# Optimization experiments

Hardware: AMD Instinct MI355X
Metric: run time of the kernel (lower is better)

Reference implementation:

```python
import jax, jax.numpy as jnp
import numpy as np

U, I, D, K, L, E = 100000, 50000, 64, 128, 2, 1250000
N = U + I
EPS = 1e-12


def setup_inputs() -> dict:
    key = jax.random.key(0)
    ks = jax.random.split(key, 8)
    return {
        "user_emb": jax.random.normal(ks[0], (U, D), jnp.float32) * 0.1,
        "item_emb": jax.random.normal(ks[1], (I, D), jnp.float32) * 0.1,
        "user_intent": jax.random.normal(ks[2], (D, K), jnp.float32) * 0.1,
        "item_intent": jax.random.normal(ks[3], (D, K), jnp.float32) * 0.1,
        "adj_vals": jax.random.uniform(ks[4], (E,), jnp.float32) * 0.1,
        "h_idx": jax.random.randint(ks[5], (E,), 0, N, jnp.int32),
        "t_idx": jax.random.randint(ks[6], (E,), 0, N, jnp.int32),
        "users": jax.random.randint(ks[7], (1024,), 0, U, jnp.int32),
        "items": jax.random.randint(jax.random.fold_in(key, 9), (1024,), 0, I, jnp.int32),
    }


def _l2norm(x):
    # torch F.normalize(p=2, dim=1): x / max(||x||_2, eps)
    n = jnp.sqrt(jnp.sum(x * x, axis=1, keepdims=True))
    return x / jnp.maximum(n, EPS)


def reference(user_emb, item_emb, user_intent, item_intent, adj_vals, h_idx, t_idx, users, items):
    n_users = user_emb.shape[0]
    n_nodes = n_users + item_emb.shape[0]

    def spmm(vals, x):
        # sparse [N,N] @ dense [N,D] via edge gather + segment-sum scatter
        return jax.ops.segment_sum(vals[:, None] * x[t_idx], h_idx, num_segments=n_nodes)

    def adaptive_vals(head, tail):
        hn, tn = _l2norm(head), _l2norm(tail)
        edge_alpha = (jnp.sum(hn * tn, axis=1) + 1.0) * 0.5  # [E]
        row_sum = jax.ops.segment_sum(edge_alpha, h_idx, num_segments=n_nodes)  # dense row-sum equivalent
        d_inv = jnp.where(row_sum > 0, 1.0 / row_sum, 0.0)
        return d_inv[h_idx] * edge_alpha  # G edge values

    all_emb = [jnp.concatenate([user_emb, item_emb], axis=0)]  # [N, D]
    gnn_list, int_list, gaa_list, iaa_list = [], [], [], []
    for _ in range(L):
        ek = all_emb[-1]
        gnn = spmm(adj_vals, ek)
        u_e, i_e = ek[:n_users], ek[n_users:]
        u_int = jax.nn.softmax(u_e @ user_intent, axis=1) @ user_intent.T
        i_int = jax.nn.softmax(i_e @ item_intent, axis=1) @ item_intent.T
        intl = jnp.concatenate([u_int, i_int], axis=0)
        g_graph = adaptive_vals(gnn[h_idx], gnn[t_idx])
        g_inten = adaptive_vals(intl[h_idx], intl[t_idx])
        gaa = spmm(g_graph, ek)
        iaa = spmm(g_inten, ek)
        gnn_list.append(gnn); int_list.append(intl)
        gaa_list.append(gaa); iaa_list.append(iaa)
        all_emb.append(gnn + intl + gaa + iaa + ek)

    final = jnp.sum(jnp.stack(all_emb, axis=1), axis=1)  # [N, D]
    ua, ia = final[:n_users], final[n_users:]
    return (ua, ia, jnp.stack(gnn_list), jnp.stack(int_list), jnp.stack(gaa_list), jnp.stack(iaa_list))
```

## Files before the change

### kernel.cpp

```cpp
#include <hip/hip_runtime.h>


#define U_CNT 100000
#define I_CNT 50000
#define D_DIM 64
#define K_DIM 128
#define L_LAYERS 2
#define E_CNT 1250000
#define N_CNT (U_CNT + I_CNT)
#define EPSF 1e-12f

#define UBLK ((U_CNT + 63) / 64)
#define IBLK ((I_CNT + 63) / 64)

#define SC_BLOCKS 256
#define SC_TPB 256
#define SC_CHUNK ((N_CNT + SC_BLOCKS - 1) / SC_BLOCKS)

typedef float vfloat4 __attribute__((ext_vector_type(4)));

__device__ __forceinline__ void nt_store4(float* p, float4 v) {
  vfloat4 nv;
  nv.x = v.x;
  nv.y = v.y;
  nv.z = v.z;
  nv.w = v.w;
  __builtin_nontemporal_store(nv, (vfloat4*)p);
}

__global__ void init_kernel(const float* __restrict__ ue, const float* __restrict__ ie,
                            float* __restrict__ ek) {
  int idx = blockIdx.x * blockDim.x + threadIdx.x;
  const int total = N_CNT * D_DIM;
  for (; idx < total; idx += gridDim.x * blockDim.x) {
    float v = (idx < U_CNT * D_DIM) ? ue[idx] : ie[idx - U_CNT * D_DIM];
    ek[idx] = v;
  }
}

__global__ void hist_kernel(const int* __restrict__ h_idx, int* __restrict__ counts) {
  int e = blockIdx.x * blockDim.x + threadIdx.x;
  for (; e < E_CNT; e += gridDim.x * blockDim.x) atomicAdd(&counts[h_idx[e]], 1);
}

__global__ void scanA_kernel(const int* __restrict__ counts, int* __restrict__ partial) {
  int b = blockIdx.x, tid = threadIdx.x, lane = tid & 63, wv = tid >> 6;
  int lo = b * SC_CHUNK;
  int hi = lo + SC_CHUNK;
  if (hi > N_CNT) hi = N_CNT;
  int s = 0;
  for (int i = lo + tid; i < hi; i += SC_TPB) s += counts[i];
#pragma unroll
  for (int off = 32; off > 0; off >>= 1) s += __shfl_xor(s, off, 64);
  __shared__ int ws[4];
  if (lane == 0) ws[wv] = s;
  __syncthreads();
  if (tid == 0) partial[b] = ws[0] + ws[1] + ws[2] + ws[3];
}

__global__ void scanB_kernel(const int* __restrict__ partial, int* __restrict__ offs) {
  int tid = threadIdx.x, lane = tid & 63, wv = tid >> 6;
  int v = partial[tid];
  int x = v;
#pragma unroll
  for (int off = 1; off < 64; off <<= 1) {
    int y = __shfl_up(x, off, 64);
    if (lane >= off) x += y;
  }
  __shared__ int wt[4];
  if (lane == 63) wt[wv] = x;
  __syncthreads();
  int add = 0;
  for (int w = 0; w < wv; w++) add += wt[w];
  offs[tid] = add + x - v;
}

__global__ void scanC_kernel(const int* __restrict__ counts, const int* __restrict__ offs,
                             int* __restrict__ row_ptr, int* __restrict__ cursor) {
  int b = blockIdx.x, tid = threadIdx.x, lane = tid & 63, wv = tid >> 6;
  __shared__ int wt[4];
  int lo = b * SC_CHUNK;
  int hi = lo + SC_CHUNK;
  if (hi > N_CNT) hi = N_CNT;
  int carry = offs[b];
  for (int base = lo; base < hi; base += SC_TPB) {
    int i = base + tid;
    int v = (i < hi) ? counts[i] : 0;
    int x = v;
#pragma unroll
    for (int off = 1; off < 64; off <<= 1) {
      int y = __shfl_up(x, off, 64);
      if (lane >= off) x += y;
    }
    if (lane == 63) wt[wv] = x;
    __syncthreads();
    int add = carry;
    for (int w = 0; w < wv; w++) add += wt[w];
    if (i < hi) {
      int e = add + x - v;
      row_ptr[i] = e;
      cursor[i] = e;
    }
    int tot = wt[0] + wt[1] + wt[2] + wt[3];
    __syncthreads();
    carry += tot;
  }
  if (b == 0 && tid == 0) row_ptr[N_CNT] = E_CNT;
}

__global__ void scatter_kernel(const int* __restrict__ h_idx, const int* __restrict__ t_idx,
                               const float* __restrict__ adj_vals, int* __restrict__ cursor,
                               int* __restrict__ t_sorted, float* __restrict__ v_sorted) {
  int e = blockIdx.x * blockDim.x + threadIdx.x;
  for (; e < E_CNT; e += gridDim.x * blockDim.x) {
    int h = h_idx[e];
    int pos = atomicAdd(&cursor[h], 1);
    t_sorted[pos] = t_idx[e];
    v_sorted[pos] = adj_vals[e];
  }
}

__global__ void transposeW_kernel(const float* __restrict__ Wu, const float* __restrict__ Wi,
                                  float* __restrict__ WuT, float* __restrict__ WiT) {
  int idx = blockIdx.x * blockDim.x + threadIdx.x;
  for (; idx < 2 * D_DIM * K_DIM; idx += gridDim.x * blockDim.x) {
    int w = idx >> 13, r = idx & (D_DIM * K_DIM - 1);
    int d = r >> 7, k = r & (K_DIM - 1);
    const float* W = w ? Wi : Wu;
    float* WT = w ? WiT : WuT;
    WT[k * D_DIM + d] = W[d * K_DIM + k];
  }
}

__global__ void spmm_gnn_kernel(const float* __restrict__ ek, const int* __restrict__ t_sorted,
                                const float* __restrict__ v_sorted,
                                const int* __restrict__ row_ptr, float* __restrict__ gnn,
                                float* __restrict__ invn_g) {
  int wv = threadIdx.x >> 6, lane = threadIdx.x & 63;
  int slot = lane >> 4, f = (lane & 15) << 2;
  int n = blockIdx.x * 4 + wv;
  if (n >= N_CNT) return;
  int start = row_ptr[n], end = row_ptr[n + 1];
  float ax = 0.f, ay = 0.f, az = 0.f, aw = 0.f;
  for (int i = start; i < end; i += 4) {
    int idx = i + slot;
    int ic = (idx < end) ? idx : (end - 1);
    int t = t_sorted[ic];
    float v = v_sorted[ic];
    if (idx >= end) v = 0.f;
    const float4 x = *(const float4*)(ek + (size_t)t * D_DIM + f);
    ax = fmaf(v, x.x, ax);
    ay = fmaf(v, x.y, ay);
    az = fmaf(v, x.z, az);
    aw = fmaf(v, x.w, aw);
  }
#pragma unroll
  for (int off = 16; off <= 32; off <<= 1) {
    ax += __shfl_xor(ax, off, 64);
    ay += __shfl_xor(ay, off, 64);
    az += __shfl_xor(az, off, 64);
    aw += __shfl_xor(aw, off, 64);
  }
  if (slot == 0) {
    float4 o = make_float4(ax, ay, az, aw);
    *(float4*)(gnn + (size_t)n * D_DIM + f) = o;
  }
  float ss = ax * ax + ay * ay + az * az + aw * aw;
#pragma unroll
  for (int off = 1; off <= 8; off <<= 1) ss += __shfl_xor(ss, off, 64);
  if (lane == 0) invn_g[n] = 1.f / fmaxf(sqrtf(ss), EPSF);
}

__global__ __launch_bounds__(256, 4) void intent_kernel(
    const float* __restrict__ ek, const float* __restrict__ Wu, const float* __restrict__ WuT,
    const float* __restrict__ Wi, const float* __restrict__ WiT, float* __restrict__ intl,
    float* __restrict__ invn_i) {
  __shared__ float buf[K_DIM * 65];
  const int tid = threadIdx.x;
  const int tx = tid & 15, ty = tid >> 4;
  const int b = blockIdx.x;
  int n0, cnt;
  const float *W, *WT;
  if (b < UBLK) {
    n0 = b * 64;
    cnt = (U_CNT - n0 < 64) ? (U_CNT - n0) : 64;
    W = Wu;
    WT = WuT;
  } else {
    n0 = U_CNT + (b - UBLK) * 64;
    cnt = (N_CNT - n0 < 64) ? (N_CNT - n0) : 64;
    W = Wi;
    WT = WiT;
  }

#pragma unroll
  for (int it = 0; it < 4; it++) {
    int idx = tid + 256 * it;
    int r = idx >> 4, q = idx & 15;
    float4 v = make_float4(0.f, 0.f, 0.f, 0.f);
    if (r < cnt) v = *(const float4*)(ek + (size_t)(n0 + r) * D_DIM + q * 4);
    buf[r * 65 + 4 * q + 0] = v.x;
    buf[r * 65 + 4 * q + 1] = v.y;
    buf[r * 65 + 4 * q + 2] = v.z;
    buf[r * 65 + 4 * q + 3] = v.w;
  }
  __syncthreads();

  float a[4][8];
#pragma unroll
  for (int i = 0; i < 4; i++)
#pragma unroll
    for (int j = 0; j < 8; j++) a[i][j] = 0.f;

  const float* wp = W + 8 * tx;
  float4 w0 = *(const float4*)(wp);
  float4 w1 = *(const float4*)(wp + 4);
  for (int d = 0; d < D_DIM; d++) {
    float4 nw0, nw1;
    if (d < D_DIM - 1) {
      nw0 = *(const float4*)(wp + (d + 1) * K_DIM);
      nw1 = *(const float4*)(wp + (d + 1) * K_DIM + 4);
    }
    float e0 = buf[(4 * ty + 0) * 65 + d];
    float e1 = buf[(4 * ty + 1) * 65 + d];
    float e2 = buf[(4 * ty + 2) * 65 + d];
    float e3 = buf[(4 * ty + 3) * 65 + d];
    float wv[8] = {w0.x, w0.y, w0.z, w0.w, w1.x, w1.y, w1.z, w1.w};
    float ev[4] = {e0, e1, e2, e3};
#pragma unroll
    for (int i = 0; i < 4; i++)
#pragma unroll
      for (int j = 0; j < 8; j++) a[i][j] = fmaf(ev[i], wv[j], a[i][j]);
    w0 = nw0;
    w1 = nw1;
  }

  float mx[4], sm[4], inv_s[4];
#pragma unroll
  for (int i = 0; i < 4; i++) {
    float m = a[i][0];
#pragma unroll
    for (int j = 1; j < 8; j++) m = fmaxf(m, a[i][j]);
    mx[i] = m;
  }
#pragma unroll
  for (int off = 1; off <= 8; off <<= 1)
#pragma unroll
    for (int i = 0; i < 4; i++) mx[i] = fmaxf(mx[i], __shfl_xor(mx[i], off, 64));
#pragma unroll
  for (int i = 0; i < 4; i++) {
    float s = 0.f;
#pragma unroll
    for (int j = 0; j < 8; j++) {
      a[i][j] = __expf(a[i][j] - mx[i]);
      s += a[i][j];
    }
    sm[i] = s;
  }
#pragma unroll
  for (int off = 1; off <= 8; off <<= 1)
#pragma unroll
    for (int i = 0; i < 4; i++) sm[i] += __shfl_xor(sm[i], off, 64);
#pragma unroll
  for (int i = 0; i < 4; i++) inv_s[i] = 1.f / sm[i];

  __syncthreads();
#pragma unroll
  for (int i = 0; i < 4; i++)
#pragma unroll
    for (int j = 0; j < 8; j++) buf[(8 * tx + j) * 65 + 4 * ty + i] = a[i][j];
  __syncthreads();

  float o[4][4];
#pragma unroll
  for (int i = 0; i < 4; i++)
#pragma unroll
    for (int j = 0; j < 4; j++) o[i][j] = 0.f;

  const float* wtp = WT + 4 * tx;
  float4 t0 = *(const float4*)(wtp);
  for (int k = 0; k < K_DIM; k++) {
    float4 nt;
    if (k < K_DIM - 1) nt = *(const float4*)(wtp + (k + 1) * D_DIM);
    float p0 = buf[k * 65 + 4 * ty + 0];
    float p1 = buf[k * 65 + 4 * ty + 1];
    float p2 = buf[k * 65 + 4 * ty + 2];
    float p3 = buf[k * 65 + 4 * ty + 3];
    float pv[4] = {p0, p1, p2, p3};
    float tv[4] = {t0.x, t0.y, t0.z, t0.w};
#pragma unroll
    for (int i = 0; i < 4; i++)
#pragma unroll
      for (int j = 0; j < 4; j++) o[i][j] = fmaf(pv[i], tv[j], o[i][j]);
    t0 = nt;
  }

  float ns[4];
#pragma unroll
  for (int i = 0; i < 4; i++) {
    float s = 0.f;
#pragma unroll
    for (int j = 0; j < 4; j++) {
      o[i][j] *= inv_s[i];
      s = fmaf(o[i][j], o[i][j], s);
    }
    ns[i] = s;
  }
#pragma unroll
  for (int off = 1; off <= 8; off <<= 1)
#pragma unroll
    for (int i = 0; i < 4; i++) ns[i] += __shfl_xor(ns[i], off, 64);
  if (tx == 0) {
#pragma unroll
    for (int i = 0; i < 4; i++) {
      int r = 4 * ty + i;
      if (r < cnt) invn_i[n0 + r] = 1.f / fmaxf(sqrtf(ns[i]), EPSF);
    }
  }
#pragma unroll
  for (int i = 0; i < 4; i++) {
    int r = 4 * ty + i;
    if (r < cnt) {
      float4 v = make_float4(o[i][0], o[i][1], o[i][2], o[i][3]);
      *(float4*)(intl + (size_t)(n0 + r) * D_DIM + 4 * tx) = v;
    }
  }
}

template <bool LAST>
__global__ void passB_kernel(const float* __restrict__ ek, const float* __restrict__ gnn,
                             const float* __restrict__ intl, const float* __restrict__ invn_g,
                             const float* __restrict__ invn_i, const int* __restrict__ t_sorted,
                             const int* __restrict__ row_ptr, float* __restrict__ gaa,
                             float* __restrict__ iaa, float* __restrict__ ek_next,
                             const float* __restrict__ ek0, float* __restrict__ fin) {
  int wv = threadIdx.x >> 6, lane = threadIdx.x & 63;
  int slot = lane >> 4, f = (lane & 15) << 2;
  int n = blockIdx.x * 4 + wv;
  if (n >= N_CNT) return;
  int start = row_ptr[n], end = row_ptr[n + 1];
  const float4 gh = *(const float4*)(gnn + (size_t)n * D_DIM + f);
  const float4 ih = *(const float4*)(intl + (size_t)n * D_DIM + f);
  float ig = invn_g[n], ii = invn_i[n];
  float rs_g = 0.f, rs_i = 0.f;
  float gx = 0.f, gy = 0.f, gz = 0.f, gw = 0.f;
  float ix = 0.f, iy = 0.f, iz = 0.f, iw = 0.f;
  for (int i = start; i < end; i += 4) {
    int idx = i + slot;
    int ic = (idx < end) ? idx : (end - 1);
    int t = t_sorted[ic];
    size_t rb = (size_t)t * D_DIM + f;
    const float4 gt = *(const float4*)(gnn + rb);
    const float4 it = *(const float4*)(intl + rb);
    const float4 et = *(const float4*)(ek + rb);
    float ivg = invn_g[t];
    float ivi = invn_i[t];
    float dg = gh.x * gt.x + gh.y * gt.y + gh.z * gt.z + gh.w * gt.w;
    float di = ih.x * it.x + ih.y * it.y + ih.z * it.z + ih.w * it.w;
#pragma unroll
    for (int off = 1; off <= 8; off <<= 1) {
      dg += __shfl_xor(dg, off, 64);
      di += __shfl_xor(di, off, 64);
    }
    float ag = fmaf(dg * ig, ivg, 1.f) * 0.5f;
    float ai = fmaf(di * ii, ivi, 1.f) * 0.5f;
    if (idx >= end) { ag = 0.f; ai = 0.f; }
    rs_g += ag;
    rs_i += ai;
    gx = fmaf(ag, et.x, gx);
    gy = fmaf(ag, et.y, gy);
    gz = fmaf(ag, et.z, gz);
    gw = fmaf(ag, et.w, gw);
    ix = fmaf(ai, et.x, ix);
    iy = fmaf(ai, et.y, iy);
    iz = fmaf(ai, et.z, iz);
    iw = fmaf(ai, et.w, iw);
  }
#pragma unroll
  for (int off = 16; off <= 32; off <<= 1) {
    rs_g += __shfl_xor(rs_g, off, 64);
    rs_i += __shfl_xor(rs_i, off, 64);
    gx += __shfl_xor(gx, off, 64);
    gy += __shfl_xor(gy, off, 64);
    gz += __shfl_xor(gz, off, 64);
    gw += __shfl_xor(gw, off, 64);
    ix += __shfl_xor(ix, off, 64);
    iy += __shfl_xor(iy, off, 64);
    iz += __shfl_xor(iz, off, 64);
    iw += __shfl_xor(iw, off, 64);
  }
  float dgi = (rs_g > 0.f) ? 1.f / rs_g : 0.f;
  float dii = (rs_i > 0.f) ? 1.f / rs_i : 0.f;
  if (slot == 0) {
    size_t ob = (size_t)n * D_DIM + f;
    float4 ga = make_float4(gx * dgi, gy * dgi, gz * dgi, gw * dgi);
    float4 ia = make_float4(ix * dii, iy * dii, iz * dii, iw * dii);
    nt_store4(gaa + ob, ga);
    nt_store4(iaa + ob, ia);
    const float4 eh = *(const float4*)(ek + ob);
    float4 en = make_float4(gh.x + ih.x + ga.x + ia.x + eh.x, gh.y + ih.y + ga.y + ia.y + eh.y,
                            gh.z + ih.z + ga.z + ia.z + eh.z, gh.w + ih.w + ga.w + ia.w + eh.w);
    if (LAST) {
      const float4 e0 = *(const float4*)(ek0 + ob);
      float4 fo = make_float4(e0.x + eh.x + en.x, e0.y + eh.y + en.y, e0.z + eh.z + en.z,
                              e0.w + eh.w + en.w);
      nt_store4(fin + ob, fo);
    } else {
      *(float4*)(ek_next + ob) = en;
    }
  }
}

extern "C" void kernel_launch(void* const* d_in, const int* in_sizes, int n_in, void* d_out,
                              int out_size, void* d_ws, size_t ws_size, hipStream_t stream) {
  const float* user_emb = (const float*)d_in[0];
  const float* item_emb = (const float*)d_in[1];
  const float* user_intent = (const float*)d_in[2];
  const float* item_intent = (const float*)d_in[3];
  const float* adj_vals = (const float*)d_in[4];
  const int* h_idx = (const int*)d_in[5];
  const int* t_idx = (const int*)d_in[6];

  float* out = (float*)d_out;
  float* fin = out;
  float* gnn_base = out + (size_t)N_CNT * D_DIM;
  float* intl_base = gnn_base + (size_t)L_LAYERS * N_CNT * D_DIM;
  float* gaa_base = intl_base + (size_t)L_LAYERS * N_CNT * D_DIM;
  float* iaa_base = gaa_base + (size_t)L_LAYERS * N_CNT * D_DIM;

  float* ws = (float*)d_ws;
  float* ekA = ws;
  float* ekB = ekA + (size_t)N_CNT * D_DIM;
  float* ekC = ekB + (size_t)N_CNT * D_DIM;
  float* v_sorted = ekC + (size_t)N_CNT * D_DIM;
  float* invn_g = v_sorted + E_CNT;
  float* invn_i = invn_g + N_CNT;
  int* t_sorted = (int*)(invn_i + N_CNT);
  int* row_ptr = t_sorted + E_CNT;
  int* counts = row_ptr + (N_CNT + 1);
  int* cursor = counts + N_CNT;
  int* partial = cursor + N_CNT;
  int* offs = partial + SC_BLOCKS;
  float* wtu = (float*)(offs + SC_BLOCKS);
  float* wti = wtu + (size_t)D_DIM * K_DIM;

  (void)hipMemsetAsync(counts, 0, N_CNT * sizeof(int), stream);
  init_kernel<<<2048, 256, 0, stream>>>(user_emb, item_emb, ekA);
  hist_kernel<<<2048, 256, 0, stream>>>(h_idx, counts);
  transposeW_kernel<<<32, 512, 0, stream>>>(user_intent, item_intent, wtu, wti);
  scanA_kernel<<<SC_BLOCKS, SC_TPB, 0, stream>>>(counts, partial);
  scanB_kernel<<<1, SC_BLOCKS, 0, stream>>>(partial, offs);
  scanC_kernel<<<SC_BLOCKS, SC_TPB, 0, stream>>>(counts, offs, row_ptr, cursor);
  scatter_kernel<<<2048, 256, 0, stream>>>(h_idx, t_idx, adj_vals, cursor, t_sorted, v_sorted);

  const int nodeBlocks = (N_CNT + 3) / 4;
  const int intentBlocks = UBLK + IBLK;

  float* ek = ekA;
  float* ekn = ekB;
  for (int l = 0; l < L_LAYERS; l++) {
    float* gnn = gnn_base + (size_t)l * N_CNT * D_DIM;
    float* intl = intl_base + (size_t)l * N_CNT * D_DIM;
    float* gaa = gaa_base + (size_t)l * N_CNT * D_DIM;
    float* iaa = iaa_base + (size_t)l * N_CNT * D_DIM;
    spmm_gnn_kernel<<<nodeBlocks, 256, 0, stream>>>(ek, t_sorted, v_sorted, row_ptr, gnn, invn_g);
    intent_kernel<<<intentBlocks, 256, 0, stream>>>(ek, user_intent, wtu, item_intent, wti, intl,
                                                    invn_i);
    if (l == L_LAYERS - 1) {
      passB_kernel<true><<<nodeBlocks, 256, 0, stream>>>(ek, gnn, intl, invn_g, invn_i, t_sorted,
                                                         row_ptr, gaa, iaa, nullptr, ekA, fin);
    } else {
      passB_kernel<false><<<nodeBlocks, 256, 0, stream>>>(ek, gnn, intl, invn_g, invn_i, t_sorted,
                                                          row_ptr, gaa, iaa, ekn, nullptr, nullptr);
      float* tmp = ek;
      ek = ekn;
      ekn = (l == 0) ? ekC : tmp;
    }
  }
}
```

Baseline: 1.145 ms.

## Fuse SpMM and intent kernels into one launch, pack edge index/value pairs

Merges the gnn SpMM and intent-projection kernels into a single horizontally fused launch, where each group of 17 blocks gives 16 blocks to SpMM rows and one block to an intent tile, so the two independent phases overlap on the GPU. Edge targets and values are packed into one int2 array so each edge needs one 8-byte load instead of two separate loads. Shared memory in the intent path is halved by staging the softmax probabilities in two 64-wide halves, which should allow higher occupancy. The costs are extra syncthreads in the intent path and passB now reading 8-byte entries when it only needs the index.

```diff
diff --git a/kernel.cpp b/kernel.cpp
--- a/kernel.cpp
+++ b/kernel.cpp
@@ -12,6 +12,9 @@
 
 #define UBLK ((U_CNT + 63) / 64)
 #define IBLK ((I_CNT + 63) / 64)
+#define NODEBLK ((N_CNT + 3) / 4)
+#define INTBLK (UBLK + IBLK)
+#define GRP 17
 
 #define SC_BLOCKS 256
 #define SC_TPB 256
@@ -110,13 +113,12 @@
 
 __global__ void scatter_kernel(const int* __restrict__ h_idx, const int* __restrict__ t_idx,
                                const float* __restrict__ adj_vals, int* __restrict__ cursor,
-                               int* __restrict__ t_sorted, float* __restrict__ v_sorted) {
+                               int2* __restrict__ tv_sorted) {
   int e = blockIdx.x * blockDim.x + threadIdx.x;
   for (; e < E_CNT; e += gridDim.x * blockDim.x) {
     int h = h_idx[e];
     int pos = atomicAdd(&cursor[h], 1);
-    t_sorted[pos] = t_idx[e];
-    v_sorted[pos] = adj_vals[e];
+    tv_sorted[pos] = make_int2(t_idx[e], __float_as_int(adj_vals[e]));
   }
 }
 
@@ -132,62 +134,68 @@
   }
 }
 
-__global__ void spmm_gnn_kernel(const float* __restrict__ ek, const int* __restrict__ t_sorted,
-                                const float* __restrict__ v_sorted,
-                                const int* __restrict__ row_ptr, float* __restrict__ gnn,
-                                float* __restrict__ invn_g) {
-  int wv = threadIdx.x >> 6, lane = threadIdx.x & 63;
-  int slot = lane >> 4, f = (lane & 15) << 2;
-  int n = blockIdx.x * 4 + wv;
-  if (n >= N_CNT) return;
-  int start = row_ptr[n], end = row_ptr[n + 1];
-  float ax = 0.f, ay = 0.f, az = 0.f, aw = 0.f;
-  for (int i = start; i < end; i += 4) {
-    int idx = i + slot;
-    int ic = (idx < end) ? idx : (end - 1);
-    int t = t_sorted[ic];
-    float v = v_sorted[ic];
-    if (idx >= end) v = 0.f;
-    const float4 x = *(const float4*)(ek + (size_t)t * D_DIM + f);
-    ax = fmaf(v, x.x, ax);
-    ay = fmaf(v, x.y, ay);
-    az = fmaf(v, x.z, az);
-    aw = fmaf(v, x.w, aw);
-  }
-#pragma unroll
-  for (int off = 16; off <= 32; off <<= 1) {
-    ax += __shfl_xor(ax, off, 64);
-    ay += __shfl_xor(ay, off, 64);
-    az += __shfl_xor(az, off, 64);
-    aw += __shfl_xor(aw, off, 64);
-  }
-  if (slot == 0) {
-    float4 o = make_float4(ax, ay, az, aw);
-    *(float4*)(gnn + (size_t)n * D_DIM + f) = o;
-  }
-  float ss = ax * ax + ay * ay + az * az + aw * aw;
-#pragma unroll
-  for (int off = 1; off <= 8; off <<= 1) ss += __shfl_xor(ss, off, 64);
-  if (lane == 0) invn_g[n] = 1.f / fmaxf(sqrtf(ss), EPSF);
-}
-
-__global__ __launch_bounds__(256, 4) void intent_kernel(
-    const float* __restrict__ ek, const float* __restrict__ Wu, const float* __restrict__ WuT,
-    const float* __restrict__ Wi, const float* __restrict__ WiT, float* __restrict__ intl,
-    float* __restrict__ invn_i) {
-  __shared__ float buf[K_DIM * 65];
+__global__ __launch_bounds__(256, 4) void phase1_kernel(
+    const float* __restrict__ ek, const int2* __restrict__ tv_sorted,
+    const int* __restrict__ row_ptr, float* __restrict__ gnn, float* __restrict__ invn_g,
+    const float* __restrict__ Wu, const float* __restrict__ WuT, const float* __restrict__ Wi,
+    const float* __restrict__ WiT, float* __restrict__ intl, float* __restrict__ invn_i) {
+  __shared__ float buf[D_DIM * 65];
+  const int bid = blockIdx.x;
+  const int grp = bid / GRP, role = bid % GRP;
+
+  if (role < 16) {
+    int sb = grp * 16 + role;
+    if (sb >= NODEBLK) return;
+    int wv = threadIdx.x >> 6, lane = threadIdx.x & 63;
+    int slot = lane >> 4, f = (lane & 15) << 2;
+    int n = sb * 4 + wv;
+    if (n >= N_CNT) return;
+    int start = row_ptr[n], end = row_ptr[n + 1];
+    float ax = 0.f, ay = 0.f, az = 0.f, aw = 0.f;
+    for (int i = start; i < end; i += 4) {
+      int idx = i + slot;
+      int ic = (idx < end) ? idx : (end - 1);
+      int2 tvv = tv_sorted[ic];
+      int t = tvv.x;
+      float v = __int_as_float(tvv.y);
+      if (idx >= end) v = 0.f;
+      const float4 x = *(const float4*)(ek + (size_t)t * D_DIM + f);
+      ax = fmaf(v, x.x, ax);
+      ay = fmaf(v, x.y, ay);
+      az = fmaf(v, x.z, az);
+      aw = fmaf(v, x.w, aw);
+    }
+#pragma unroll
+    for (int off = 16; off <= 32; off <<= 1) {
+      ax += __shfl_xor(ax, off, 64);
+      ay += __shfl_xor(ay, off, 64);
+      az += __shfl_xor(az, off, 64);
+      aw += __shfl_xor(aw, off, 64);
+    }
+    if (slot == 0) {
+      float4 o = make_float4(ax, ay, az, aw);
+      *(float4*)(gnn + (size_t)n * D_DIM + f) = o;
+    }
+    float ss = ax * ax + ay * ay + az * az + aw * aw;
+#pragma unroll
+    for (int off = 1; off <= 8; off <<= 1) ss += __shfl_xor(ss, off, 64);
+    if (lane == 0) invn_g[n] = 1.f / fmaxf(sqrtf(ss), EPSF);
+    return;
+  }
+
+  int ib = grp;
+  if (ib >= INTBLK) return;
   const int tid = threadIdx.x;
   const int tx = tid & 15, ty = tid >> 4;
-  const int b = blockIdx.x;
   int n0, cnt;
   const float *W, *WT;
-  if (b < UBLK) {
-    n0 = b * 64;
+  if (ib < UBLK) {
+    n0 = ib * 64;
     cnt = (U_CNT - n0 < 64) ? (U_CNT - n0) : 64;
     W = Wu;
     WT = WuT;
   } else {
-    n0 = U_CNT + (b - UBLK) * 64;
+    n0 = U_CNT + (ib - UBLK) * 64;
     cnt = (N_CNT - n0 < 64) ? (N_CNT - n0) : 64;
     W = Wi;
     WT = WiT;
@@ -264,35 +272,41 @@
 #pragma unroll
   for (int i = 0; i < 4; i++) inv_s[i] = 1.f / sm[i];
 
-  __syncthreads();
+  float o[4][4];
 #pragma unroll
   for (int i = 0; i < 4; i++)
 #pragma unroll
-    for (int j = 0; j < 8; j++) buf[(8 * tx + j) * 65 + 4 * ty + i] = a[i][j];
-  __syncthreads();
-
-  float o[4][4];
-#pragma unroll
-  for (int i = 0; i < 4; i++)
-#pragma unroll
     for (int j = 0; j < 4; j++) o[i][j] = 0.f;
 
   const float* wtp = WT + 4 * tx;
-  float4 t0 = *(const float4*)(wtp);
-  for (int k = 0; k < K_DIM; k++) {
-    float4 nt;
-    if (k < K_DIM - 1) nt = *(const float4*)(wtp + (k + 1) * D_DIM);
-    float p0 = buf[k * 65 + 4 * ty + 0];
-    float p1 = buf[k * 65 + 4 * ty + 1];
-    float p2 = buf[k * 65 + 4 * ty + 2];
-    float p3 = buf[k * 65 + 4 * ty + 3];
-    float pv[4] = {p0, p1, p2, p3};
-    float tv[4] = {t0.x, t0.y, t0.z, t0.w};
-#pragma unroll
-    for (int i = 0; i < 4; i++)
-#pragma unroll
-      for (int j = 0; j < 4; j++) o[i][j] = fmaf(pv[i], tv[j], o[i][j]);
-    t0 = nt;
+#pragma unroll
+  for (int half = 0; half < 2; half++) {
+    __syncthreads();
+    if ((tx >> 3) == half) {
+      int txh = tx & 7;
+#pragma unroll
+      for (int i = 0; i < 4; i++)
+#pragma unroll
+        for (int j = 0; j < 8; j++) buf[(8 * txh + j) * 65 + 4 * ty + i] = a[i][j];
+    }
+    __syncthreads();
+    const float* wth = wtp + (half ? 64 * D_DIM : 0);
+    float4 t0 = *(const float4*)(wth);
+    for (int k = 0; k < 64; k++) {
+      float4 nt;
+      if (k < 63) nt = *(const float4*)(wth + (k + 1) * D_DIM);
+      float p0 = buf[k * 65 + 4 * ty + 0];
+      float p1 = buf[k * 65 + 4 * ty + 1];
+      float p2 = buf[k * 65 + 4 * ty + 2];
+      float p3 = buf[k * 65 + 4 * ty + 3];
+      float pv[4] = {p0, p1, p2, p3};
+      float tv[4] = {t0.x, t0.y, t0.z, t0.w};
+#pragma unroll
+      for (int i = 0; i < 4; i++)
+#pragma unroll
+        for (int j = 0; j < 4; j++) o[i][j] = fmaf(pv[i], tv[j], o[i][j]);
+      t0 = nt;
+    }
   }
 
   float ns[4];
@@ -330,7 +344,7 @@
 template <bool LAST>
 __global__ void passB_kernel(const float* __restrict__ ek, const float* __restrict__ gnn,
                              const float* __restrict__ intl, const float* __restrict__ invn_g,
-                             const float* __restrict__ invn_i, const int* __restrict__ t_sorted,
+                             const float* __restrict__ invn_i, const int2* __restrict__ tv_sorted,
                              const int* __restrict__ row_ptr, float* __restrict__ gaa,
                              float* __restrict__ iaa, float* __restrict__ ek_next,
                              const float* __restrict__ ek0, float* __restrict__ fin) {
@@ -348,7 +362,7 @@
   for (int i = start; i < end; i += 4) {
     int idx = i + slot;
     int ic = (idx < end) ? idx : (end - 1);
-    int t = t_sorted[ic];
+    int t = tv_sorted[ic].x;
     size_t rb = (size_t)t * D_DIM + f;
     const float4 gt = *(const float4*)(gnn + rb);
     const float4 it = *(const float4*)(intl + rb);
@@ -432,11 +446,10 @@
   float* ekA = ws;
   float* ekB = ekA + (size_t)N_CNT * D_DIM;
   float* ekC = ekB + (size_t)N_CNT * D_DIM;
-  float* v_sorted = ekC + (size_t)N_CNT * D_DIM;
-  float* invn_g = v_sorted + E_CNT;
+  int2* tv_sorted = (int2*)(ekC + (size_t)N_CNT * D_DIM);
+  float* invn_g = (float*)(tv_sorted + E_CNT);
   float* invn_i = invn_g + N_CNT;
-  int* t_sorted = (int*)(invn_i + N_CNT);
-  int* row_ptr = t_sorted + E_CNT;
+  int* row_ptr = (int*)(invn_i + N_CNT);
   int* counts = row_ptr + (N_CNT + 1);
   int* cursor = counts + N_CNT;
   int* partial = cursor + N_CNT;
@@ -451,10 +464,9 @@
   scanA_kernel<<<SC_BLOCKS, SC_TPB, 0, stream>>>(counts, partial);
   scanB_kernel<<<1, SC_BLOCKS, 0, stream>>>(partial, offs);
   scanC_kernel<<<SC_BLOCKS, SC_TPB, 0, stream>>>(counts, offs, row_ptr, cursor);
-  scatter_kernel<<<2048, 256, 0, stream>>>(h_idx, t_idx, adj_vals, cursor, t_sorted, v_sorted);
-
-  const int nodeBlocks = (N_CNT + 3) / 4;
-  const int intentBlocks = UBLK + IBLK;
+  scatter_kernel<<<2048, 256, 0, stream>>>(h_idx, t_idx, adj_vals, cursor, tv_sorted);
+
+  const int phase1Blocks = INTBLK * GRP;
 
   float* ek = ekA;
   float* ekn = ekB;
@@ -463,15 +475,15 @@
     float* intl = intl_base + (size_t)l * N_CNT * D_DIM;
     float* gaa = gaa_base + (size_t)l * N_CNT * D_DIM;
     float* iaa = iaa_base + (size_t)l * N_CNT * D_DIM;
-    spmm_gnn_kernel<<<nodeBlocks, 256, 0, stream>>>(ek, t_sorted, v_sorted, row_ptr, gnn, invn_g);
-    intent_kernel<<<intentBlocks, 256, 0, stream>>>(ek, user_intent, wtu, item_intent, wti, intl,
+    phase1_kernel<<<phase1Blocks, 256, 0, stream>>>(ek, tv_sorted, row_ptr, gnn, invn_g,
+                                                    user_intent, wtu, item_intent, wti, intl,
                                                     invn_i);
     if (l == L_LAYERS - 1) {
-      passB_kernel<true><<<nodeBlocks, 256, 0, stream>>>(ek, gnn, intl, invn_g, invn_i, t_sorted,
-                                                         row_ptr, gaa, iaa, nullptr, ekA, fin);
+      passB_kernel<true><<<NODEBLK, 256, 0, stream>>>(ek, gnn, intl, invn_g, invn_i, tv_sorted,
+                                                      row_ptr, gaa, iaa, nullptr, ekA, fin);
     } else {
-      passB_kernel<false><<<nodeBlocks, 256, 0, stream>>>(ek, gnn, intl, invn_g, invn_i, t_sorted,
-                                                          row_ptr, gaa, iaa, ekn, nullptr, nullptr);
+      passB_kernel<false><<<NODEBLK, 256, 0, stream>>>(ek, gnn, intl, invn_g, invn_i, tv_sorted,
+                                                       row_ptr, gaa, iaa, ekn, nullptr, nullptr);
       float* tmp = ek;
       ek = ekn;
       ekn = (l == 0) ? ekC : tmp;
```

Result: slower. 1.211 ms (+5.7%).
